# Kernel optimization log

Measured on AMD Instinct MI355X. Metric: run time of the kernel, lower is better.

## Reference

```python
import jax, jax.numpy as jnp
import numpy as np

B, T, K, H, NH = 16, 2048, 128, 1024, 8
NEG = -jnp.inf


def _ln(x, g, b, eps=1e-5):
    m = x.mean(-1, keepdims=True)
    v = ((x - m) ** 2).mean(-1, keepdims=True)
    return (x - m) * jax.lax.rsqrt(v + eps) * g + b


def _mha(q, k, v, in_w, in_b, out_w, out_b, nh, bias):
    # torch nn.MultiheadAttention (batch_first, eval mode). bias: additive mask (B or 1, 1, Lq, Lk)
    Bq, Lq, Hd = q.shape
    Lk = k.shape[1]
    d = Hd // nh
    wq, wk, wv = in_w[:Hd], in_w[Hd:2 * Hd], in_w[2 * Hd:]
    bq, bk, bv = in_b[:Hd], in_b[Hd:2 * Hd], in_b[2 * Hd:]
    qh = (q @ wq.T + bq).reshape(Bq, Lq, nh, d).transpose(0, 2, 1, 3)
    kh = (k @ wk.T + bk).reshape(Bq, Lk, nh, d).transpose(0, 2, 1, 3)
    vh = (v @ wv.T + bv).reshape(Bq, Lk, nh, d).transpose(0, 2, 1, 3)
    scores = jnp.einsum('bhqd,bhkd->bhqk', qh, kh) * (1.0 / np.sqrt(d)) + bias
    attn = jax.nn.softmax(scores, axis=-1)
    o = jnp.einsum('bhqk,bhkd->bhqd', attn, vh).transpose(0, 2, 1, 3).reshape(Bq, Lq, Hd)
    return o @ out_w.T + out_b


def setup_inputs() -> dict:
    key = jax.random.key(0)
    ks = jax.random.split(key, 12)
    projected = jax.random.normal(ks[0], (B, T, H), dtype=jnp.float32)
    starts = jnp.sort(jax.random.randint(ks[1], (B, K), 0, T - 1), axis=-1)
    widths = jax.random.randint(ks[2], (B, K), 1, 33)
    ends = jnp.minimum(starts + widths, T)
    boundaries = jnp.stack([starts, ends], axis=-1).astype(jnp.int64)
    slot_mask = jnp.ones((B, K), dtype=jnp.float32)
    s = 0.02
    p = {
        'qp_w': jax.random.normal(ks[3], (H, H)) * s, 'qp_b': jnp.zeros((H,)),
        'ca_in_w': jax.random.normal(ks[4], (3 * H, H)) * s, 'ca_in_b': jnp.zeros((3 * H,)),
        'ca_out_w': jax.random.normal(ks[5], (H, H)) * s, 'ca_out_b': jnp.zeros((H,)),
        'cn_g': jnp.ones((H,)), 'cn_b': jnp.zeros((H,)),
        'sa_in_w': jax.random.normal(ks[6], (3 * H, H)) * s, 'sa_in_b': jnp.zeros((3 * H,)),
        'sa_out_w': jax.random.normal(ks[7], (H, H)) * s, 'sa_out_b': jnp.zeros((H,)),
        'on_g': jnp.ones((H,)), 'on_b': jnp.zeros((H,)),
    }
    return {'projected': projected, 'boundaries': boundaries, 'slot_mask': slot_mask, **p}


def reference(projected, boundaries, slot_mask, qp_w, qp_b, ca_in_w, ca_in_b, ca_out_w, ca_out_b,
              cn_g, cn_b, sa_in_w, sa_in_b, sa_out_w, sa_out_b, on_g, on_b):
    Bb, Tt, Hh = projected.shape
    Kk = slot_mask.shape[1]
    tidx = jnp.arange(Tt)
    starts = boundaries[:, :, 0]  # (B,K)
    ends = boundaries[:, :, 1]
    # in-boundary membership: (B,K,T)
    in_bkt = (tidx[None, None, :] >= starts[:, :, None]) & (tidx[None, None, :] < ends[:, :, None])
    valid = slot_mask > 0.5  # (B,K)
    # --- mean-pool init queries ---
    in_slot = (in_bkt & (slot_mask[:, :, None] > 0)).astype(projected.dtype)  # (B,K,T)
    w = in_slot / jnp.clip(in_slot.sum(axis=-1, keepdims=True), 1.0, None)
    init_slots = jnp.einsum('bkt,bth->bkh', w, projected)
    queries = init_slots @ qp_w.T + qp_b
    # --- boundary-masked cross attention (True = blocked) ---
    blocked = ~(in_bkt & valid[:, :, None])  # (B,K,T)
    cross_bias = jnp.where(blocked, NEG, 0.0)[:, None, :, :]  # (B,1,K,T)
    attn_out = _mha(queries, projected, projected, ca_in_w, ca_in_b, ca_out_w, ca_out_b, NH, cross_bias)
    slots = _ln(attn_out + queries, cn_g, cn_b)
    # --- causal self-attention over slots with key padding ---
    causal = jnp.where(jnp.triu(jnp.ones((Kk, Kk), bool), 1), NEG, 0.0)[None, None, :, :]
    pad = jnp.where(slot_mask[:, None, None, :] < 0.5, NEG, 0.0)  # (B,1,1,K)
    ctx = _mha(slots, slots, slots, sa_in_w, sa_in_b, sa_out_w, sa_out_b, NH, causal + pad)
    return _ln(ctx + slots, on_g, on_b)
```

## Files before the change

kernel.cpp:

```cpp
#include <hip/hip_runtime.h>
#include <hip/hip_bf16.h>


#define Bc 16
#define Tc 2048
#define Kc 128
#define Hc 1024
#define NHc 8

typedef unsigned short u16;
typedef __attribute__((ext_vector_type(8))) short short8v;
typedef __attribute__((ext_vector_type(4))) float f32x4;

__device__ __forceinline__ float bf2f(u16 u){ return __uint_as_float(((unsigned)u)<<16); }
__device__ __forceinline__ u16 f2bf(float f){
  unsigned x = __float_as_uint(f);
  return (u16)((x + 0x7fffu + ((x>>16)&1u)) >> 16);
}
__device__ __forceinline__ float4 ld4(const float* p){ return *(const float4*)p; }
__device__ __forceinline__ float ldx(const void* x, size_t idx, bool isbf){
  return isbf ? bf2f(((const u16*)x)[idx]) : ((const float*)x)[idx];
}
__device__ __forceinline__ bool probe_bf(const u16* probe){ return probe[0] == 0x3F80; }

__device__ __forceinline__ void gload_lds16(const u16* g, u16* l){
  __builtin_amdgcn_global_load_lds(
      (const __attribute__((address_space(1))) unsigned int*)g,
      (__attribute__((address_space(3))) unsigned int*)l, 16, 0, 0);
}

__device__ __forceinline__ short8v pack8(float4 f0, float4 f1){
  short8v v;
  v[0]=(short)f2bf(f0.x); v[1]=(short)f2bf(f0.y);
  v[2]=(short)f2bf(f0.z); v[3]=(short)f2bf(f0.w);
  v[4]=(short)f2bf(f1.x); v[5]=(short)f2bf(f1.y);
  v[6]=(short)f2bf(f1.z); v[7]=(short)f2bf(f1.w);
  return v;
}

struct CvtArgs { const void* src[15]; int n[15]; long long off[15]; int tobf[15]; };

__global__ __launch_bounds__(256) void convert_params(CvtArgs a, float* fbase,
                                                      u16* bbase, const u16* probe)
{
  bool isbf = probe_bf(probe);
  int g = blockIdx.x*256 + threadIdx.x;
  int stride = gridDim.x*256;
  #pragma unroll 1
  for (int seg=0; seg<15; seg++){
    int n = a.n[seg];
    const void* s = a.src[seg];
    if (a.tobf[seg]){
      u16* d = bbase + a.off[seg];
      if (isbf){ const u16* su=(const u16*)s; for (int i=g;i<n;i+=stride) d[i]=su[i]; }
      else     { const float* sf=(const float*)s; for (int i=g;i<n;i+=stride) d[i]=f2bf(sf[i]); }
    } else {
      float* d = fbase + a.off[seg];
      for (int i=g;i<n;i+=stride) d[i] = ldx(s, i, isbf);
    }
  }
}

__global__ __launch_bounds__(256) void transpose_bf(
    const u16* __restrict__ src, u16* __restrict__ dst, int n)
{
  __shared__ u16 t[32][33];
  int bx = blockIdx.x*32, by = blockIdx.y*32;
  int tx = threadIdx.x & 31, ty = threadIdx.x >> 5;
  #pragma unroll
  for (int i=0;i<32;i+=8)
    t[ty+i][tx] = src[(size_t)(by+ty+i)*n + bx+tx];
  __syncthreads();
  #pragma unroll
  for (int i=0;i<32;i+=8)
    dst[(size_t)(bx+ty+i)*n + by+tx] = t[tx][ty+i];
}

__global__ __launch_bounds__(256) void gemm_mfma(
    const u16* __restrict__ A, const u16* __restrict__ W,
    const float* __restrict__ bias, float* __restrict__ Cf, u16* __restrict__ Cb,
    int M, int N, int Kd, int lda, int ldw, int ldc, float alpha,
    int ZH, long long sAb, long long sAh, long long sWb, long long sWh,
    long long sCb, long long sCh, long long sBh)
{
  __shared__ __align__(16) u16 As[128*32];
  __shared__ __align__(16) u16 Bs[128*32];
  int z = blockIdx.z, bi = z / ZH, hi = z % ZH;
  A += (size_t)bi*sAb + (size_t)hi*sAh;
  W += (size_t)bi*sWb + (size_t)hi*sWh;
  int tid = threadIdx.x;
  int m0 = blockIdx.y*128, n0 = blockIdx.x*128;
  int wave = tid >> 6, lane = tid & 63;
  int wm = (wave >> 1)*64, wn = (wave & 1)*64;
  int r = lane & 15, half = lane >> 4;
  int srow = wave*32 + (lane >> 2);
  int skc  = (lane & 3) << 3;
  u16* ldsA = &As[wave*1024];
  u16* ldsB = &Bs[wave*1024];

  f32x4 acc[4][4] = {};

  for (int k0 = 0; k0 < Kd; k0 += 32){
    gload_lds16(A + (size_t)(m0+srow   )*lda + k0 + skc, ldsA);
    gload_lds16(A + (size_t)(m0+srow+16)*lda + k0 + skc, ldsA + 512);
    gload_lds16(W + (size_t)(n0+srow   )*ldw + k0 + skc, ldsB);
    gload_lds16(W + (size_t)(n0+srow+16)*ldw + k0 + skc, ldsB + 512);
    __syncthreads();
    short8v a[4], b[4];
    #pragma unroll
    for (int mi=0;mi<4;mi++)
      a[mi] = *(const short8v*)&As[(wm+mi*16+r)*32 + half*8];
    #pragma unroll
    for (int ni=0;ni<4;ni++)
      b[ni] = *(const short8v*)&Bs[(wn+ni*16+r)*32 + half*8];
    #pragma unroll
    for (int mi=0;mi<4;mi++)
      #pragma unroll
      for (int ni=0;ni<4;ni++)
        acc[mi][ni] = __builtin_amdgcn_mfma_f32_16x16x32_bf16(a[mi], b[ni], acc[mi][ni], 0, 0, 0);
    __syncthreads();
  }

  float* Cfp = Cf ? Cf + (size_t)bi*sCb + (size_t)hi*sCh : nullptr;
  u16*   Cbp = Cb ? Cb + (size_t)bi*sCb + (size_t)hi*sCh : nullptr;
  #pragma unroll
  for (int ni=0;ni<4;ni++){
    int col = n0 + wn + ni*16 + r;
    float bvv = bias ? bias[(size_t)hi*sBh + col] : 0.f;
    #pragma unroll
    for (int mi=0;mi<4;mi++){
      #pragma unroll
      for (int d=0;d<4;d++){
        int rowc = m0 + wm + mi*16 + half*4 + d;
        float o = alpha*acc[mi][ni][d] + bvv;
        if (Cfp) Cfp[(size_t)rowc*ldc + col] = o;
        if (Cbp) Cbp[(size_t)rowc*ldc + col] = f2bf(o);
      }
    }
  }
}

__global__ __launch_bounds__(256) void gemm_mfma64(
    const u16* __restrict__ A, const u16* __restrict__ W,
    const float* __restrict__ bias, float* __restrict__ Cf, u16* __restrict__ Cb,
    int M, int N, int Kd, int lda, int ldw, int ldc, float alpha,
    int ZH, long long sAb, long long sAh, long long sWb, long long sWh,
    long long sCb, long long sCh, long long sBh)
{
  __shared__ __align__(16) u16 As[128*32];
  __shared__ __align__(16) u16 Bs[64*32];
  int z = blockIdx.z, bi = z / ZH, hi = z % ZH;
  A += (size_t)bi*sAb + (size_t)hi*sAh;
  W += (size_t)bi*sWb + (size_t)hi*sWh;
  int tid = threadIdx.x;
  int m0 = blockIdx.y*128, n0 = blockIdx.x*64;
  int wave = tid >> 6, lane = tid & 63;
  int wm = (wave >> 1)*64, wn = (wave & 1)*32;
  int r = lane & 15, half = lane >> 4;
  int srow = wave*32 + (lane >> 2);
  int brow = wave*16 + (lane >> 2);
  int skc  = (lane & 3) << 3;
  u16* ldsA = &As[wave*1024];
  u16* ldsB = &Bs[wave*512];

  f32x4 acc[4][2] = {};

  for (int k0 = 0; k0 < Kd; k0 += 32){
    gload_lds16(A + (size_t)(m0+srow   )*lda + k0 + skc, ldsA);
    gload_lds16(A + (size_t)(m0+srow+16)*lda + k0 + skc, ldsA + 512);
    gload_lds16(W + (size_t)(n0+brow   )*ldw + k0 + skc, ldsB);
    __syncthreads();
    short8v a[4], b[2];
    #pragma unroll
    for (int mi=0;mi<4;mi++)
      a[mi] = *(const short8v*)&As[(wm+mi*16+r)*32 + half*8];
    #pragma unroll
    for (int ni=0;ni<2;ni++)
      b[ni] = *(const short8v*)&Bs[(wn+ni*16+r)*32 + half*8];
    #pragma unroll
    for (int mi=0;mi<4;mi++)
      #pragma unroll
      for (int ni=0;ni<2;ni++)
        acc[mi][ni] = __builtin_amdgcn_mfma_f32_16x16x32_bf16(a[mi], b[ni], acc[mi][ni], 0, 0, 0);
    __syncthreads();
  }

  float* Cfp = Cf ? Cf + (size_t)bi*sCb + (size_t)hi*sCh : nullptr;
  u16*   Cbp = Cb ? Cb + (size_t)bi*sCb + (size_t)hi*sCh : nullptr;
  #pragma unroll
  for (int ni=0;ni<2;ni++){
    int col = n0 + wn + ni*16 + r;
    float bvv = bias ? bias[(size_t)hi*sBh + col] : 0.f;
    #pragma unroll
    for (int mi=0;mi<4;mi++){
      #pragma unroll
      for (int d=0;d<4;d++){
        int rowc = m0 + wm + mi*16 + half*4 + d;
        float o = alpha*acc[mi][ni][d] + bvv;
        if (Cfp) Cfp[(size_t)rowc*ldc + col] = o;
        if (Cbp) Cbp[(size_t)rowc*ldc + col] = f2bf(o);
      }
    }
  }
}

__global__ __launch_bounds__(1024) void pool_kernel(
    const void* __restrict__ x, const int* __restrict__ bnd,
    const float* __restrict__ maskf, u16* __restrict__ out,
    const u16* __restrict__ probe)
{
  __shared__ float red[3*1024];
  bool isbf = probe_bf(probe);
  bool is64 = (bnd[1] == 0);
  int slot = blockIdx.x; int b = slot >> 7; int tid = threadIdx.x;
  int s0 = is64 ? bnd[4*slot]   : bnd[2*slot];
  int e0 = is64 ? bnd[4*slot+2] : bnd[2*slot+1];
  int rh = tid >> 8;
  int q = (tid & 255)*4;
  float acc[4] = {0.f,0.f,0.f,0.f};
  for (int t=s0+rh; t<e0; t+=4){
    size_t base = ((size_t)b*Tc + (size_t)t)*Hc + q;
    if (isbf){
      ushort4 v = *(const ushort4*)((const u16*)x + base);
      acc[0]+=bf2f(v.x); acc[1]+=bf2f(v.y); acc[2]+=bf2f(v.z); acc[3]+=bf2f(v.w);
    } else {
      float4 v = ld4((const float*)x + base);
      acc[0]+=v.x; acc[1]+=v.y; acc[2]+=v.z; acc[3]+=v.w;
    }
  }
  if (rh > 0){
    #pragma unroll
    for (int r=0;r<4;r++) red[(rh-1)*1024 + q + r] = acc[r];
  }
  __syncthreads();
  if (rh == 0){
    int cnt = e0 - s0; if (cnt < 1) cnt = 1;
    float inv = (maskf[slot] > 0.5f) ? 1.f/(float)cnt : 0.f;
    ushort4 o;
    o.x=f2bf((acc[0]+red[q+0]+red[1024+q+0]+red[2048+q+0])*inv);
    o.y=f2bf((acc[1]+red[q+1]+red[1024+q+1]+red[2048+q+1])*inv);
    o.z=f2bf((acc[2]+red[q+2]+red[1024+q+2]+red[2048+q+2])*inv);
    o.w=f2bf((acc[3]+red[q+3]+red[1024+q+3]+red[2048+q+3])*inv);
    *(ushort4*)(out + (size_t)slot*Hc + q) = o;
  }
}

__global__ __launch_bounds__(512, 2) void cross_attn4(
    const void* __restrict__ x, const int* __restrict__ bnd,
    const u16* __restrict__ Yg, u16* __restrict__ pooled,
    const u16* __restrict__ probe)
{
  __shared__ __align__(16) u16 Xs[32*1024];
  __shared__ float redC[4*2*64*4];
  __shared__ float sc[8*32];
  __shared__ __align__(16) float pt[32*8];
  bool isbf = probe_bf(probe);
  bool is64 = (bnd[1] == 0);
  int slot = blockIdx.x; int b = slot >> 7;
  int tid = threadIdx.x;
  int wv = tid >> 6, lane = tid & 63;
  int s0 = is64 ? bnd[4*slot]   : bnd[2*slot];
  int e0 = is64 ? bnd[4*slot+2] : bnd[2*slot+1];
  int w = e0 - s0;

  {
    int rrow = tid >> 7;
    int cu = (tid & 127) * 8;
    for (int t = rrow; t < w; t += 4){
      size_t base = ((size_t)b*Tc + (size_t)(s0+t))*Hc + cu;
      int dst = t*1024 + (cu ^ ((t&7)<<3));
      short8v v;
      if (isbf){
        v = *(const short8v*)((const u16*)x + base);
      } else {
        const float* xf = (const float*)x + base;
        v = pack8(ld4(xf), ld4(xf+4));
      }
      *(short8v*)&Xs[dst] = v;
    }
  }
  __syncthreads();

  if (wv < 4){
    int r = lane & 15, half = lane >> 4;
    f32x4 acc0 = {0.f,0.f,0.f,0.f}, acc1 = {0.f,0.f,0.f,0.f};
    #pragma unroll
    for (int ks=0; ks<8; ks++){
      int k = wv*256 + ks*32 + half*8;
      short8v vb = {0,0,0,0,0,0,0,0};
      if (r < 8)
        vb = *(const short8v*)(Yg + (size_t)slot*8192 + r*1024 + k);
      int xs = k ^ ((r&7)<<3);
      short8v a0 = *(const short8v*)&Xs[ r      *1024 + xs];
      short8v a1 = *(const short8v*)&Xs[(16+r)*1024 + xs];
      acc0 = __builtin_amdgcn_mfma_f32_16x16x32_bf16(a0, vb, acc0, 0, 0, 0);
      acc1 = __builtin_amdgcn_mfma_f32_16x16x32_bf16(a1, vb, acc1, 0, 0, 0);
    }
    #pragma unroll
    for (int i=0;i<4;i++){
      redC[((wv*2+0)*64+lane)*4+i] = acc0[i];
      redC[((wv*2+1)*64+lane)*4+i] = acc1[i];
    }
  }
  __syncthreads();

  {
    int f = tid >> 8, rem = tid & 255, l = rem >> 2, i = rem & 3;
    float v = 0.f;
    #pragma unroll
    for (int q=0; q<4; q++) v += redC[((q*2+f)*64+l)*4+i];
    int hh = l & 15;
    int t  = f*16 + (l>>4)*4 + i;
    if (hh < 8) sc[hh*32 + t] = v * 0.08838834764831845f;
  }
  __syncthreads();

  if (tid < 256){
    int hh = tid >> 5, t = tid & 31;
    float v = (t < w) ? sc[hh*32 + t] : -1e30f;
    float m = v;
    for (int off=16; off; off>>=1) m = fmaxf(m, __shfl_xor(m, off));
    float e = (t < w) ? __expf(v - m) : 0.f;
    float s = e;
    for (int off=16; off; off>>=1) s += __shfl_xor(s, off);
    pt[t*8 + hh] = e / s;
  }
  __syncthreads();

  {
    int d0 = tid*2;
    float pa[8][2] = {};
    for (int t=0; t<w; t++){
      float4 p0 = *(const float4*)&pt[t*8];
      float4 p1 = *(const float4*)&pt[t*8+4];
      unsigned xw = *(const unsigned*)&Xs[t*1024 + (d0 ^ ((t&7)<<3))];
      float x0 = bf2f((u16)(xw & 0xffffu));
      float x1 = bf2f((u16)(xw >> 16));
      pa[0][0]+=p0.x*x0; pa[0][1]+=p0.x*x1;
      pa[1][0]+=p0.y*x0; pa[1][1]+=p0.y*x1;
      pa[2][0]+=p0.z*x0; pa[2][1]+=p0.z*x1;
      pa[3][0]+=p0.w*x0; pa[3][1]+=p0.w*x1;
      pa[4][0]+=p1.x*x0; pa[4][1]+=p1.x*x1;
      pa[5][0]+=p1.y*x0; pa[5][1]+=p1.y*x1;
      pa[6][0]+=p1.z*x0; pa[6][1]+=p1.z*x1;
      pa[7][0]+=p1.w*x0; pa[7][1]+=p1.w*x1;
    }
    #pragma unroll
    for (int hh=0;hh<8;hh++){
      ushort2 o; o.x = f2bf(pa[hh][0]); o.y = f2bf(pa[hh][1]);
      *(ushort2*)(pooled + (size_t)slot*8192 + hh*1024 + d0) = o;
    }
  }
}

__global__ __launch_bounds__(256) void fused_sa(
    const float* __restrict__ qkv, const float* __restrict__ maskf,
    u16* __restrict__ ctx_b)
{
  __shared__ __align__(16) u16 Qs[128*128];
  __shared__ __align__(16) u16 Ks[128*128];
  __shared__ __align__(16) u16 Vs[128*128];
  __shared__ float rmax[2][128];
  __shared__ float rsum[2][128];
  __shared__ float maskL[128];
  int z = blockIdx.x;
  int b = z >> 3, h = z & 7;
  int tid = threadIdx.x;
  const float* base = qkv + (size_t)(b*128)*3072 + h*128;

  {
    int sr = tid >> 4, scol = (tid & 15) * 8;
    if (tid < 128) maskL[tid] = maskf[b*128 + tid];
    #pragma unroll
    for (int i=0;i<8;i++){
      int rr = sr + i*16;
      const float* qp = base + (size_t)rr*3072 + scol;
      int swz = scol ^ ((rr&7)<<3);
      *(short8v*)&Qs[rr*128 + swz]  = pack8(ld4(qp),      ld4(qp+4));
      *(short8v*)&Ks[rr*128 + swz]  = pack8(ld4(qp+1024), ld4(qp+1028));
      *(short8v*)&Vs[rr*128 + scol] = pack8(ld4(qp+2048), ld4(qp+2052));
    }
  }
  __syncthreads();

  int wave = tid >> 6, lane = tid & 63;
  int wr = wave >> 1, wc = wave & 1;
  int r = lane & 15, half = lane >> 4;

  f32x4 acc[4][4] = {};
  #pragma unroll
  for (int ks=0; ks<4; ks++){
    int kb = ks*32 + half*8;
    int xo = kb ^ ((r&7)<<3);
    short8v a[4], bb[4];
    #pragma unroll
    for (int mi=0;mi<4;mi++)
      a[mi] = *(const short8v*)&Qs[(wr*64+mi*16+r)*128 + xo];
    #pragma unroll
    for (int ni=0;ni<4;ni++)
      bb[ni] = *(const short8v*)&Ks[(wc*64+ni*16+r)*128 + xo];
    #pragma unroll
    for (int mi=0;mi<4;mi++)
      #pragma unroll
      for (int ni=0;ni<4;ni++)
        acc[mi][ni] = __builtin_amdgcn_mfma_f32_16x16x32_bf16(a[mi], bb[ni], acc[mi][ni], 0, 0, 0);
  }

  const float scale = 0.08838834764831845f;
  float rmx[4][4];
  #pragma unroll
  for (int mi=0;mi<4;mi++)
    #pragma unroll
    for (int d=0;d<4;d++){
      int q = wr*64 + mi*16 + half*4 + d;
      float mx = -1e30f;
      #pragma unroll
      for (int ni=0;ni<4;ni++){
        int k = wc*64 + ni*16 + r;
        float v = acc[mi][ni][d]*scale;
        if (k > q || maskL[k] < 0.5f) v = -1e30f;
        acc[mi][ni][d] = v;
        mx = fmaxf(mx, v);
      }
      for (int off=8; off; off>>=1) mx = fmaxf(mx, __shfl_xor(mx, off));
      rmx[mi][d] = mx;
      if (r == 0) rmax[wc][q] = mx;
    }
  __syncthreads();

  float rs_[4][4];
  #pragma unroll
  for (int mi=0;mi<4;mi++)
    #pragma unroll
    for (int d=0;d<4;d++){
      int q = wr*64 + mi*16 + half*4 + d;
      float m = fmaxf(rmax[0][q], rmax[1][q]);
      float s = 0.f;
      #pragma unroll
      for (int ni=0;ni<4;ni++){
        float e = __expf(acc[mi][ni][d] - m);
        acc[mi][ni][d] = e;
        s += e;
      }
      for (int off=8; off; off>>=1) s += __shfl_xor(s, off);
      rs_[mi][d] = s;
      if (r == 0) rsum[wc][q] = s;
    }
  __syncthreads();

  #pragma unroll
  for (int mi=0;mi<4;mi++)
    #pragma unroll
    for (int d=0;d<4;d++){
      int q = wr*64 + mi*16 + half*4 + d;
      float inv = 1.f / (rsum[0][q] + rsum[1][q]);
      #pragma unroll
      for (int ni=0;ni<4;ni++){
        int k = wc*64 + ni*16 + r;
        Qs[q*128 + (k ^ ((q&7)<<3))] = f2bf(acc[mi][ni][d]*inv);
      }
    }
  __syncthreads();

  f32x4 o[4][4] = {};
  #pragma unroll
  for (int ks=0; ks<4; ks++){
    int kb = ks*32 + half*8;
    int xo = kb ^ ((r&7)<<3);
    short8v a[4], bb[4];
    #pragma unroll
    for (int mi=0;mi<4;mi++)
      a[mi] = *(const short8v*)&Qs[(wr*64+mi*16+r)*128 + xo];
    #pragma unroll
    for (int ni=0;ni<4;ni++){
      int col = wc*64 + ni*16 + r;
      short8v t;
      #pragma unroll
      for (int j=0;j<8;j++) t[j] = (short)Vs[(kb + j)*128 + col];
      bb[ni] = t;
    }
    #pragma unroll
    for (int mi=0;mi<4;mi++)
      #pragma unroll
      for (int ni=0;ni<4;ni++)
        o[mi][ni] = __builtin_amdgcn_mfma_f32_16x16x32_bf16(a[mi], bb[ni], o[mi][ni], 0, 0, 0);
  }

  #pragma unroll
  for (int ni=0;ni<4;ni++){
    int d = wc*64 + ni*16 + r;
    #pragma unroll
    for (int mi=0;mi<4;mi++){
      #pragma unroll
      for (int dd=0;dd<4;dd++){
        int q = wr*64 + mi*16 + half*4 + dd;
        ctx_b[(size_t)(b*128+q)*1024 + h*128 + d] = f2bf(o[mi][ni][dd]);
      }
    }
  }
}

__global__ __launch_bounds__(256) void ln_res(
    const float* __restrict__ xin, const float* __restrict__ res,
    const float* __restrict__ g, const float* __restrict__ bb,
    float* __restrict__ outf, u16* __restrict__ outb, const u16* __restrict__ probe,
    u16* __restrict__ dualb)
{
  __shared__ float red[256];
  bool tobf = (probe != nullptr) && probe_bf(probe);
  int row = blockIdx.x, tid = threadIdx.x;
  const float* xr = xin + (size_t)row*1024;
  const float* rr = res + (size_t)row*1024;
  float v[4]; float s = 0.f;
  #pragma unroll
  for (int r=0;r<4;r++){ v[r] = xr[tid+256*r] + rr[tid+256*r]; s += v[r]; }
  red[tid] = s; __syncthreads();
  for (int off=128; off>0; off>>=1){ if (tid<off) red[tid]+=red[tid+off]; __syncthreads(); }
  float mean = red[0] * (1.f/1024.f);
  __syncthreads();
  float s2 = 0.f;
  #pragma unroll
  for (int r=0;r<4;r++){ float d = v[r]-mean; s2 += d*d; }
  red[tid]=s2; __syncthreads();
  for (int off=128; off>0; off>>=1){ if (tid<off) red[tid]+=red[tid+off]; __syncthreads(); }
  float var = red[0]*(1.f/1024.f);
  float rs = rsqrtf(var + 1e-5f);
  #pragma unroll
  for (int r=0;r<4;r++){
    int c = tid+256*r;
    float o = (v[r]-mean)*rs*g[c] + bb[c];
    if (tobf) outb[(size_t)row*1024 + c] = f2bf(o);
    else      outf[(size_t)row*1024 + c] = o;
    if (dualb) dualb[(size_t)row*1024 + c] = f2bf(o);
  }
}

extern "C" void kernel_launch(void* const* d_in, const int* in_sizes, int n_in,
                              void* d_out, int out_size, void* d_ws, size_t ws_size,
                              hipStream_t stream)
{
  const void* x       = d_in[0];
  const int* bnd      = (const int*)d_in[1];
  const u16* probe    = (const u16*)d_in[9];
  float* ws = (float*)d_ws;

  const long long F_qp_b    = 0;
  const long long F_ca_in_b = 1024;
  const long long F_ca_out_b= 4096;
  const long long F_cn_g    = 5120;
  const long long F_cn_b    = 6144;
  const long long F_sa_in_b = 7168;
  const long long F_sa_out_b= 10240;
  const long long F_on_g    = 11264;
  const long long F_on_b    = 12288;
  const long long F_smask   = 13312;
  u16* wb = (u16*)(ws + 15360);
  const long long B_qp_w    = 0;
  const long long B_ca_in_w = 1048576;
  const long long B_ca_out_w= 4194304;
  const long long B_sa_in_w = 5242880;
  const long long B_sa_out_w= 8388608;
  const long long B_wkT     = 9437184;
  const long long PB        = 5258240;

  float* qbuf    = ws + PB + 0;
  float* slots   = ws + PB + 2097152;
  u16*   Ybuf    = (u16*)(ws + PB + 4194304);
  u16*   poolb   = Ybuf;
  u16*   islots  = (u16*)(ws + PB + 12582912);
  u16*   qbuf_b  = (u16*)(ws + PB + 13631488);
  u16*   qhbuf   = (u16*)(ws + PB + 14680064);
  u16*   attnb   = (u16*)(ws + PB + 15728640);
  float* attn2   = ws + PB + 16777216;
  u16*   slots_b = (u16*)(ws + PB + 18874368);
  float* qkv     = ws + PB + 19922944;
  u16*   ctx_b   = (u16*)(ws + PB + 28311552);
  float* ctx2    = ws + PB + 29360128;
  if (ws_size < (size_t)(PB + 31457280ll) * 4ull) return;

  CvtArgs ca;
  const int srcIdx[15]     = {3,5,7,11,13, 4,6,8,9,10,12,14,15,16, 2};
  const long long offs[15] = {B_qp_w,B_ca_in_w,B_ca_out_w,B_sa_in_w,B_sa_out_w,
                              F_qp_b,F_ca_in_b,F_ca_out_b,F_cn_g,F_cn_b,
                              F_sa_in_b,F_sa_out_b,F_on_g,F_on_b,F_smask};
  const int tobf[15]       = {1,1,1,1,1, 0,0,0,0,0,0,0,0,0, 0};
  for (int i=0;i<15;i++){ ca.src[i]=d_in[srcIdx[i]]; ca.n[i]=in_sizes[srcIdx[i]];
                          ca.off[i]=offs[i]; ca.tobf[i]=tobf[i]; }
  convert_params<<<dim3(4096),dim3(256),0,stream>>>(ca, ws, wb, probe);

  const float* Pf = ws;
  transpose_bf<<<dim3(32,32),dim3(256),0,stream>>>(wb + B_ca_in_w + 1048576ll,
      wb + B_wkT, 1024);
  pool_kernel<<<dim3(2048),dim3(1024),0,stream>>>(x, bnd, Pf+F_smask, islots, probe);
  gemm_mfma64<<<dim3(16,16,1),dim3(256),0,stream>>>(islots, wb+B_qp_w, Pf+F_qp_b,
      qbuf, qbuf_b,
      2048,1024,1024, 1024,1024,1024, 1.f, 1, 0,0, 0,0, 0,0, 0);
  gemm_mfma64<<<dim3(16,16,1),dim3(256),0,stream>>>(qbuf_b, wb+B_ca_in_w, Pf+F_ca_in_b,
      (float*)nullptr, qhbuf,
      2048,1024,1024, 1024,1024,1024, 1.f, 1, 0,0, 0,0, 0,0, 0);
  gemm_mfma<<<dim3(8,16,8),dim3(256),0,stream>>>(qhbuf, wb+B_wkT,
      (const float*)nullptr, (float*)nullptr, Ybuf,
      2048,1024,128, 1024,1024,8192, 1.f, 8, 0,128, 0,128, 0,1024, 0);
  cross_attn4<<<dim3(2048),dim3(512),0,stream>>>(x, bnd, Ybuf, poolb, probe);
  gemm_mfma64<<<dim3(2,16,8),dim3(256),0,stream>>>(poolb, wb+B_ca_in_w+2097152ll,
      Pf+F_ca_in_b+2048, (float*)nullptr, attnb,
      2048,128,1024, 8192,1024,1024, 1.f, 8, 0,1024, 0,131072, 0,128, 128);
  gemm_mfma64<<<dim3(16,16,1),dim3(256),0,stream>>>(attnb, wb+B_ca_out_w, Pf+F_ca_out_b,
      attn2, (u16*)nullptr,
      2048,1024,1024, 1024,1024,1024, 1.f, 1, 0,0, 0,0, 0,0, 0);
  ln_res<<<dim3(2048),dim3(256),0,stream>>>(attn2, qbuf, Pf+F_cn_g, Pf+F_cn_b,
      slots, (u16*)nullptr, (const u16*)nullptr, slots_b);
  gemm_mfma64<<<dim3(48,16,1),dim3(256),0,stream>>>(slots_b, wb+B_sa_in_w, Pf+F_sa_in_b,
      qkv, (u16*)nullptr,
      2048,3072,1024, 1024,1024,3072, 1.f, 1, 0,0, 0,0, 0,0, 0);
  fused_sa<<<dim3(128),dim3(256),0,stream>>>(qkv, Pf+F_smask, ctx_b);
  gemm_mfma64<<<dim3(16,16,1),dim3(256),0,stream>>>(ctx_b, wb+B_sa_out_w, Pf+F_sa_out_b,
      ctx2, (u16*)nullptr,
      2048,1024,1024, 1024,1024,1024, 1.f, 1, 0,0, 0,0, 0,0, 0);
  ln_res<<<dim3(2048),dim3(256),0,stream>>>(ctx2, slots, Pf+F_on_g, Pf+F_on_b,
      (float*)d_out, (u16*)d_out, probe, (u16*)nullptr);
}
```

Before: 485.5 us.

## Widen pool loads, use direct global-to-LDS loads, split self-attention by query halves

The pool kernel now has each thread sum 8 contiguous values with 16-byte loads over 8 row groups, and the reduction goes through a larger shared buffer. Cross-attention loads bf16 input rows straight into LDS with a gload_lds16 helper using an XOR swizzle. Self-attention is split into two blocks per (batch, head), one per 64-query half, with K and V sharing one LDS buffer loaded in turn, which doubles the grid and cuts LDS per block. The aim is more parallelism and fewer instructions, at the cost of recomputing K/V staging per block and an extra sync.

```diff
diff --git a/kernel.cpp b/kernel.cpp
--- a/kernel.cpp
+++ b/kernel.cpp
@@ -209,43 +209,47 @@
     const float* __restrict__ maskf, u16* __restrict__ out,
     const u16* __restrict__ probe)
 {
-  __shared__ float red[3*1024];
+  __shared__ float red[8*1024];
   bool isbf = probe_bf(probe);
   bool is64 = (bnd[1] == 0);
   int slot = blockIdx.x; int b = slot >> 7; int tid = threadIdx.x;
   int s0 = is64 ? bnd[4*slot]   : bnd[2*slot];
   int e0 = is64 ? bnd[4*slot+2] : bnd[2*slot+1];
-  int rh = tid >> 8;
-  int q = (tid & 255)*4;
-  float acc[4] = {0.f,0.f,0.f,0.f};
-  for (int t=s0+rh; t<e0; t+=4){
-    size_t base = ((size_t)b*Tc + (size_t)t)*Hc + q;
+  int g = tid >> 7;
+  int c = (tid & 127)*8;
+  float acc[8] = {};
+  for (int t=s0+g; t<e0; t+=8){
+    size_t base = ((size_t)b*Tc + (size_t)t)*Hc + c;
     if (isbf){
-      ushort4 v = *(const ushort4*)((const u16*)x + base);
-      acc[0]+=bf2f(v.x); acc[1]+=bf2f(v.y); acc[2]+=bf2f(v.z); acc[3]+=bf2f(v.w);
+      short8v v = *(const short8v*)((const u16*)x + base);
+      #pragma unroll
+      for (int j=0;j<8;j++) acc[j] += bf2f((u16)v[j]);
     } else {
-      float4 v = ld4((const float*)x + base);
-      acc[0]+=v.x; acc[1]+=v.y; acc[2]+=v.z; acc[3]+=v.w;
-    }
-  }
-  if (rh > 0){
-    #pragma unroll
-    for (int r=0;r<4;r++) red[(rh-1)*1024 + q + r] = acc[r];
-  }
-  __syncthreads();
-  if (rh == 0){
+      float4 f0 = ld4((const float*)x + base), f1 = ld4((const float*)x + base + 4);
+      acc[0]+=f0.x; acc[1]+=f0.y; acc[2]+=f0.z; acc[3]+=f0.w;
+      acc[4]+=f1.x; acc[5]+=f1.y; acc[6]+=f1.z; acc[7]+=f1.w;
+    }
+  }
+  #pragma unroll
+  for (int j=0;j<8;j++) red[g*1024 + c + j] = acc[j];
+  __syncthreads();
+  if (tid < 256){
+    int d0 = tid*4;
     int cnt = e0 - s0; if (cnt < 1) cnt = 1;
     float inv = (maskf[slot] > 0.5f) ? 1.f/(float)cnt : 0.f;
+    float s[4] = {0.f,0.f,0.f,0.f};
+    #pragma unroll
+    for (int g2=0; g2<8; g2++){
+      s[0]+=red[g2*1024+d0+0]; s[1]+=red[g2*1024+d0+1];
+      s[2]+=red[g2*1024+d0+2]; s[3]+=red[g2*1024+d0+3];
+    }
     ushort4 o;
-    o.x=f2bf((acc[0]+red[q+0]+red[1024+q+0]+red[2048+q+0])*inv);
-    o.y=f2bf((acc[1]+red[q+1]+red[1024+q+1]+red[2048+q+1])*inv);
-    o.z=f2bf((acc[2]+red[q+2]+red[1024+q+2]+red[2048+q+2])*inv);
-    o.w=f2bf((acc[3]+red[q+3]+red[1024+q+3]+red[2048+q+3])*inv);
-    *(ushort4*)(out + (size_t)slot*Hc + q) = o;
-  }
-}
-
-__global__ __launch_bounds__(512, 2) void cross_attn4(
+    o.x=f2bf(s[0]*inv); o.y=f2bf(s[1]*inv); o.z=f2bf(s[2]*inv); o.w=f2bf(s[3]*inv);
+    *(ushort4*)(out + (size_t)slot*Hc + d0) = o;
+  }
+}
+
+__global__ __launch_bounds__(512, 2) void cross_attn5(
     const void* __restrict__ x, const int* __restrict__ bnd,
     const u16* __restrict__ Yg, u16* __restrict__ pooled,
     const u16* __restrict__ probe)
@@ -263,20 +267,22 @@
   int e0 = is64 ? bnd[4*slot+2] : bnd[2*slot+1];
   int w = e0 - s0;
 
-  {
+  if (isbf){
+    for (int t = wv; t < w; t += 8){
+      const u16* g = (const u16*)x + ((size_t)b*Tc + (size_t)(s0+t))*Hc;
+      u16* l = &Xs[t*1024];
+      int sw = t & 7;
+      gload_lds16(g + (((lane     ) ^ sw) << 3), l);
+      gload_lds16(g + (((lane + 64) ^ sw) << 3), l + 512);
+    }
+  } else {
     int rrow = tid >> 7;
     int cu = (tid & 127) * 8;
     for (int t = rrow; t < w; t += 4){
       size_t base = ((size_t)b*Tc + (size_t)(s0+t))*Hc + cu;
       int dst = t*1024 + (cu ^ ((t&7)<<3));
-      short8v v;
-      if (isbf){
-        v = *(const short8v*)((const u16*)x + base);
-      } else {
-        const float* xf = (const float*)x + base;
-        v = pack8(ld4(xf), ld4(xf+4));
-      }
-      *(short8v*)&Xs[dst] = v;
+      const float* xf = (const float*)x + base;
+      *(short8v*)&Xs[dst] = pack8(ld4(xf), ld4(xf+4));
     }
   }
   __syncthreads();
@@ -353,18 +359,17 @@
   }
 }
 
-__global__ __launch_bounds__(256) void fused_sa(
+__global__ __launch_bounds__(256) void fused_sa2(
     const float* __restrict__ qkv, const float* __restrict__ maskf,
     u16* __restrict__ ctx_b)
 {
-  __shared__ __align__(16) u16 Qs[128*128];
-  __shared__ __align__(16) u16 Ks[128*128];
-  __shared__ __align__(16) u16 Vs[128*128];
-  __shared__ float rmax[2][128];
-  __shared__ float rsum[2][128];
+  __shared__ __align__(16) u16 Qs[64*128];
+  __shared__ __align__(16) u16 KVs[128*128];
+  __shared__ float rmax[4][64];
+  __shared__ float rsum[4][64];
   __shared__ float maskL[128];
   int z = blockIdx.x;
-  int b = z >> 3, h = z & 7;
+  int b = z >> 4, h = (z >> 1) & 7, qp = z & 1;
   int tid = threadIdx.x;
   const float* base = qkv + (size_t)(b*128)*3072 + h*128;
 
@@ -372,79 +377,79 @@
     int sr = tid >> 4, scol = (tid & 15) * 8;
     if (tid < 128) maskL[tid] = maskf[b*128 + tid];
     #pragma unroll
+    for (int i=0;i<4;i++){
+      int rr = sr + i*16;
+      const float* qpp = base + (size_t)(qp*64+rr)*3072 + scol;
+      *(short8v*)&Qs[rr*128 + (scol ^ ((rr&7)<<3))] = pack8(ld4(qpp), ld4(qpp+4));
+    }
+    #pragma unroll
     for (int i=0;i<8;i++){
       int rr = sr + i*16;
-      const float* qp = base + (size_t)rr*3072 + scol;
-      int swz = scol ^ ((rr&7)<<3);
-      *(short8v*)&Qs[rr*128 + swz]  = pack8(ld4(qp),      ld4(qp+4));
-      *(short8v*)&Ks[rr*128 + swz]  = pack8(ld4(qp+1024), ld4(qp+1028));
-      *(short8v*)&Vs[rr*128 + scol] = pack8(ld4(qp+2048), ld4(qp+2052));
+      const float* kp = base + (size_t)rr*3072 + 1024 + scol;
+      *(short8v*)&KVs[rr*128 + (scol ^ ((rr&7)<<3))] = pack8(ld4(kp), ld4(kp+4));
     }
   }
   __syncthreads();
 
   int wave = tid >> 6, lane = tid & 63;
-  int wr = wave >> 1, wc = wave & 1;
   int r = lane & 15, half = lane >> 4;
 
-  f32x4 acc[4][4] = {};
+  f32x4 acc[4][2] = {};
   #pragma unroll
   for (int ks=0; ks<4; ks++){
     int kb = ks*32 + half*8;
     int xo = kb ^ ((r&7)<<3);
-    short8v a[4], bb[4];
-    #pragma unroll
-    for (int mi=0;mi<4;mi++)
-      a[mi] = *(const short8v*)&Qs[(wr*64+mi*16+r)*128 + xo];
-    #pragma unroll
-    for (int ni=0;ni<4;ni++)
-      bb[ni] = *(const short8v*)&Ks[(wc*64+ni*16+r)*128 + xo];
-    #pragma unroll
-    for (int mi=0;mi<4;mi++)
-      #pragma unroll
-      for (int ni=0;ni<4;ni++)
+    short8v a[4], bb[2];
+    #pragma unroll
+    for (int mi=0;mi<4;mi++)
+      a[mi] = *(const short8v*)&Qs[(mi*16+r)*128 + xo];
+    #pragma unroll
+    for (int ni=0;ni<2;ni++)
+      bb[ni] = *(const short8v*)&KVs[(wave*32+ni*16+r)*128 + xo];
+    #pragma unroll
+    for (int mi=0;mi<4;mi++)
+      #pragma unroll
+      for (int ni=0;ni<2;ni++)
         acc[mi][ni] = __builtin_amdgcn_mfma_f32_16x16x32_bf16(a[mi], bb[ni], acc[mi][ni], 0, 0, 0);
   }
 
   const float scale = 0.08838834764831845f;
-  float rmx[4][4];
   #pragma unroll
   for (int mi=0;mi<4;mi++)
     #pragma unroll
     for (int d=0;d<4;d++){
-      int q = wr*64 + mi*16 + half*4 + d;
+      int ql = mi*16 + half*4 + d;
+      int qg = qp*64 + ql;
       float mx = -1e30f;
       #pragma unroll
-      for (int ni=0;ni<4;ni++){
-        int k = wc*64 + ni*16 + r;
+      for (int ni=0;ni<2;ni++){
+        int k = wave*32 + ni*16 + r;
         float v = acc[mi][ni][d]*scale;
-        if (k > q || maskL[k] < 0.5f) v = -1e30f;
+        if (k > qg || maskL[k] < 0.5f) v = -1e30f;
         acc[mi][ni][d] = v;
         mx = fmaxf(mx, v);
       }
       for (int off=8; off; off>>=1) mx = fmaxf(mx, __shfl_xor(mx, off));
-      rmx[mi][d] = mx;
-      if (r == 0) rmax[wc][q] = mx;
-    }
-  __syncthreads();
-
-  float rs_[4][4];
+      if (r == 0) rmax[wave][ql] = mx;
+    }
+  __syncthreads();
+
   #pragma unroll
   for (int mi=0;mi<4;mi++)
     #pragma unroll
     for (int d=0;d<4;d++){
-      int q = wr*64 + mi*16 + half*4 + d;
-      float m = fmaxf(rmax[0][q], rmax[1][q]);
+      int ql = mi*16 + half*4 + d;
+      float m = fmaxf(fmaxf(rmax[0][ql], rmax[1][ql]),
+                      fmaxf(rmax[2][ql], rmax[3][ql]));
       float s = 0.f;
       #pragma unroll
-      for (int ni=0;ni<4;ni++){
+      for (int ni=0;ni<2;ni++){
         float e = __expf(acc[mi][ni][d] - m);
         acc[mi][ni][d] = e;
         s += e;
       }
       for (int off=8; off; off>>=1) s += __shfl_xor(s, off);
-      rs_[mi][d] = s;
-      if (r == 0) rsum[wc][q] = s;
+      if (r == 0) rsum[wave][ql] = s;
     }
   __syncthreads();
 
@@ -452,49 +457,60 @@
   for (int mi=0;mi<4;mi++)
     #pragma unroll
     for (int d=0;d<4;d++){
-      int q = wr*64 + mi*16 + half*4 + d;
-      float inv = 1.f / (rsum[0][q] + rsum[1][q]);
-      #pragma unroll
-      for (int ni=0;ni<4;ni++){
-        int k = wc*64 + ni*16 + r;
-        Qs[q*128 + (k ^ ((q&7)<<3))] = f2bf(acc[mi][ni][d]*inv);
+      int ql = mi*16 + half*4 + d;
+      float inv = 1.f / (rsum[0][ql]+rsum[1][ql]+rsum[2][ql]+rsum[3][ql]);
+      #pragma unroll
+      for (int ni=0;ni<2;ni++){
+        int k = wave*32 + ni*16 + r;
+        Qs[ql*128 + (k ^ ((ql&7)<<3))] = f2bf(acc[mi][ni][d]*inv);
       }
     }
   __syncthreads();
 
-  f32x4 o[4][4] = {};
+  {
+    int sr = tid >> 4, scol = (tid & 15) * 8;
+    #pragma unroll
+    for (int i=0;i<8;i++){
+      int rr = sr + i*16;
+      const float* vp = base + (size_t)rr*3072 + 2048 + scol;
+      *(short8v*)&KVs[rr*128 + scol] = pack8(ld4(vp), ld4(vp+4));
+    }
+  }
+  __syncthreads();
+
+  f32x4 o[4][2] = {};
   #pragma unroll
   for (int ks=0; ks<4; ks++){
     int kb = ks*32 + half*8;
     int xo = kb ^ ((r&7)<<3);
-    short8v a[4], bb[4];
-    #pragma unroll
-    for (int mi=0;mi<4;mi++)
-      a[mi] = *(const short8v*)&Qs[(wr*64+mi*16+r)*128 + xo];
-    #pragma unroll
-    for (int ni=0;ni<4;ni++){
-      int col = wc*64 + ni*16 + r;
+    short8v a[4], bb[2];
+    #pragma unroll
+    for (int mi=0;mi<4;mi++)
+      a[mi] = *(const short8v*)&Qs[(mi*16+r)*128 + xo];
+    #pragma unroll
+    for (int ni=0;ni<2;ni++){
+      int col = wave*32 + ni*16 + r;
       short8v t;
       #pragma unroll
-      for (int j=0;j<8;j++) t[j] = (short)Vs[(kb + j)*128 + col];
+      for (int j=0;j<8;j++) t[j] = (short)KVs[(kb + j)*128 + col];
       bb[ni] = t;
     }
     #pragma unroll
     for (int mi=0;mi<4;mi++)
       #pragma unroll
-      for (int ni=0;ni<4;ni++)
+      for (int ni=0;ni<2;ni++)
         o[mi][ni] = __builtin_amdgcn_mfma_f32_16x16x32_bf16(a[mi], bb[ni], o[mi][ni], 0, 0, 0);
   }
 
   #pragma unroll
-  for (int ni=0;ni<4;ni++){
-    int d = wc*64 + ni*16 + r;
+  for (int ni=0;ni<2;ni++){
+    int d = wave*32 + ni*16 + r;
     #pragma unroll
     for (int mi=0;mi<4;mi++){
       #pragma unroll
       for (int dd=0;dd<4;dd++){
-        int q = wr*64 + mi*16 + half*4 + dd;
-        ctx_b[(size_t)(b*128+q)*1024 + h*128 + d] = f2bf(o[mi][ni][dd]);
+        int ql = mi*16 + half*4 + dd;
+        ctx_b[(size_t)(b*128 + qp*64 + ql)*1024 + h*128 + d] = f2bf(o[mi][ni][dd]);
       }
     }
   }
@@ -601,7 +617,7 @@
   gemm_mfma<<<dim3(8,16,8),dim3(256),0,stream>>>(qhbuf, wb+B_wkT,
       (const float*)nullptr, (float*)nullptr, Ybuf,
       2048,1024,128, 1024,1024,8192, 1.f, 8, 0,128, 0,128, 0,1024, 0);
-  cross_attn4<<<dim3(2048),dim3(512),0,stream>>>(x, bnd, Ybuf, poolb, probe);
+  cross_attn5<<<dim3(2048),dim3(512),0,stream>>>(x, bnd, Ybuf, poolb, probe);
   gemm_mfma64<<<dim3(2,16,8),dim3(256),0,stream>>>(poolb, wb+B_ca_in_w+2097152ll,
       Pf+F_ca_in_b+2048, (float*)nullptr, attnb,
       2048,128,1024, 8192,1024,1024, 1.f, 8, 0,1024, 0,131072, 0,128, 128);
@@ -613,7 +629,7 @@
   gemm_mfma64<<<dim3(48,16,1),dim3(256),0,stream>>>(slots_b, wb+B_sa_in_w, Pf+F_sa_in_b,
       qkv, (u16*)nullptr,
       2048,3072,1024, 1024,1024,3072, 1.f, 1, 0,0, 0,0, 0,0, 0);
-  fused_sa<<<dim3(128),dim3(256),0,stream>>>(qkv, Pf+F_smask, ctx_b);
+  fused_sa2<<<dim3(256),dim3(256),0,stream>>>(qkv, Pf+F_smask, ctx_b);
   gemm_mfma64<<<dim3(16,16,1),dim3(256),0,stream>>>(ctx_b, wb+B_sa_out_w, Pf+F_sa_out_b,
       ctx2, (u16*)nullptr,
       2048,1024,1024, 1024,1024,1024, 1.f, 1, 0,0, 0,0, 0,0, 0);
```

Result: no change. 481.9 us (-0.7%).
